# Optimization experiments

Hardware: AMD Instinct MI355X
Metric: run time of the kernel (lower is better)

Reference implementation:

```python
import jax, jax.numpy as jnp
import numpy as np

EPS = 1e-5  # torch BatchNorm1d default eps
N0, N, ORIG, F, K, H, NC = 16, 96, 92, 64, 41, 128, 3


def _bn(x, g, b, axes):
    # training-mode batchnorm: biased batch stats over `axes`, per-channel affine
    m = jnp.mean(x, axis=axes, keepdims=True)
    v = jnp.mean((x - m) ** 2, axis=axes, keepdims=True)
    return (x - m) / jnp.sqrt(v + EPS) * g + b


def setup_inputs() -> dict:
    key = jax.random.key(0)
    ks = jax.random.split(key, 16)
    s = 0.05
    return {
        "atom_fea": jax.random.normal(ks[0], (N0, N, ORIG), jnp.float32),
        "nbr_fea": jax.random.normal(ks[1], (N0, N, N, K), jnp.float32),
        "adj": jax.random.randint(ks[2], (N0, N, N), 0, 2, jnp.int64),
        "emb_W": jax.random.normal(ks[3], (ORIG, F), jnp.float32) * s,
        "emb_b": jnp.zeros((F,), jnp.float32),
        "conv_W": jax.random.normal(ks[4], (NC, 2 * F + K, 2 * F), jnp.float32) * s,
        "conv_b": jnp.zeros((NC, 2 * F), jnp.float32),
        "bn1_g": jnp.ones((NC, 2 * F), jnp.float32),
        "bn1_b": jnp.zeros((NC, 2 * F), jnp.float32),
        "bn2_g": jnp.ones((NC, F), jnp.float32),
        "bn2_b": jnp.zeros((NC, F), jnp.float32),
        "fc_W": jax.random.normal(ks[5], (F, H), jnp.float32) * s,
        "fc_b": jnp.zeros((H,), jnp.float32),
        "out_W": jax.random.normal(ks[6], (H, 1), jnp.float32) * s,
        "out_b": jnp.zeros((1,), jnp.float32),
    }


def reference(atom_fea, nbr_fea, adj, emb_W, emb_b, conv_W, conv_b,
              bn1_g, bn1_b, bn2_g, bn2_b, fc_W, fc_b, out_W, out_b):
    fea = atom_fea @ emb_W + emb_b                       # (N0, N, F)
    adjf = adj.astype(fea.dtype)[..., None]              # (N0, N, N, 1)
    for i in range(NC):
        # NOTE: faithful to source - both FEA and masked term broadcast atom j's
        # own features along the neighbor axis (unsqueeze(2) in torch code).
        FEA = jnp.broadcast_to(fea[:, :, None, :], (N0, N, N, F))
        total = jnp.concatenate([FEA, adjf * FEA, nbr_fea], axis=3)   # (N0,N,N,2F+K)
        gated = total @ conv_W[i] + conv_b[i]                         # (N0,N,N,2F)
        gated = _bn(gated, bn1_g[i], bn1_b[i], (0, 1, 2))
        filt, core = jnp.split(gated, 2, axis=3)
        summed = jnp.sum(jax.nn.sigmoid(filt) * jax.nn.softplus(core), axis=2)  # (N0,N,F)
        summed = _bn(summed, bn2_g[i], bn2_b[i], (0, 1))
        fea = jax.nn.softplus(fea + summed)
    crys = jnp.mean(fea, axis=1)                                      # (N0, F)
    crys = jax.nn.softplus(jax.nn.softplus(crys) @ fc_W + fc_b)       # (N0, H)
    return crys @ out_W + out_b                                       # (N0, 1)
```

## Files before the change

### kernel.cpp

```cpp
#include <hip/hip_runtime.h>
#include <math.h>

#define N0c   16
#define NAt   96
#define ORIG  92
#define Fc    64
#define Kc    41
#define Hc    128
#define NCc   3
#define C2    128
#define EPSBN 1e-5f
#define JG    4
#define JPW   (NAt / JG)
#define NREP  32
#define SRL_STRIDE 12288
#define AROW  72
#define WFRAG 16384
#define INV1  (1.f / (float)(N0c * NAt * NAt))
#define INV2  (1.f / (float)(N0c * NAt))

typedef __attribute__((ext_vector_type(8))) short short8_t;
typedef __attribute__((ext_vector_type(4))) float f32x4;

__device__ __forceinline__ float sp_(float x){
    return fmaxf(x, 0.f) + __logf(1.f + __expf(-fabsf(x)));
}
__device__ __forceinline__ float sgm_(float x){
    return 1.f / (1.f + __expf(-x));
}
__device__ __forceinline__ unsigned short bfhi(float x){
    union { float f; unsigned u; } v; v.f = x;
    unsigned r = v.u + 0x7fff + ((v.u >> 16) & 1);
    return (unsigned short)(r >> 16);
}
__device__ __forceinline__ float bf2f(unsigned short h){
    union { float f; unsigned u; } v; v.u = ((unsigned)h) << 16; return v.f;
}

__global__ __launch_bounds__(256) void k_pre(const float* __restrict__ nbr,
                                             const int*   __restrict__ adj,
                                             float* __restrict__ ST,
                                             float* __restrict__ cntf){
    int r    = blockIdx.x;
    int lane = threadIdx.x & 63;
    int jg   = __builtin_amdgcn_readfirstlane(threadIdx.x >> 6);
    __shared__ float rS[JG][Kc], rT[JG][Kc], rc[JG];
    float S = 0.f, T = 0.f, cn = 0.f;
    int j0 = jg * JPW;
    for (int j = j0; j < j0 + JPW; ++j){
        float a = (float)adj[r * NAt + j];
        float v = (lane < Kc) ? nbr[((size_t)r * NAt + j) * Kc + lane] : 0.f;
        S += v; T += a * v; cn += a;
    }
    if (lane < Kc){ rS[jg][lane] = S; rT[jg][lane] = T; }
    if (lane == 0) rc[jg] = cn;
    __syncthreads();
    int t = threadIdx.x;
    if (t < Kc){
        ST[r * (2 * Kc) + t]      = rS[0][t] + rS[1][t] + rS[2][t] + rS[3][t];
        ST[r * (2 * Kc) + Kc + t] = rT[0][t] + rT[1][t] + rT[2][t] + rT[3][t];
    }
    if (t == 0) cntf[r] = rc[0] + rc[1] + rc[2] + rc[3];
}

__global__ __launch_bounds__(128) void k_gram(const float* __restrict__ nbr,
                                              const int*   __restrict__ adj,
                                              float* __restrict__ pG,
                                              float* __restrict__ ST,
                                              float* __restrict__ cntf,
                                              float* __restrict__ G,
                                              int rpb, int doST){
    int blk = blockIdx.x;
    int t   = threadIdx.x;
    int k   = (t % 21) * 2;
    int lb  = (t / 21) * 7;
    __shared__ float L[NAt * Kc];
    __shared__ float AJf[NAt];
    if (blk == 0){
        for (int i = t; i < Kc * Kc; i += 128) G[i] = 0.f;
    }
    float a0[7] = {0,0,0,0,0,0,0}, a1[7] = {0,0,0,0,0,0,0};
    for (int rr = 0; rr < rpb; ++rr){
        int r = blk * rpb + rr;
        __syncthreads();
        for (int i = t; i < NAt * Kc; i += 128)
            L[i] = nbr[(size_t)r * NAt * Kc + i];
        if (t < NAt) AJf[t] = (float)adj[r * NAt + t];
        __syncthreads();
        if (doST && t < Kc){
            float S = 0.f, T = 0.f;
            for (int j = 0; j < NAt; ++j){
                float v = L[j * Kc + t];
                S += v; T += AJf[j] * v;
            }
            ST[r * (2 * Kc) + t]      = S;
            ST[r * (2 * Kc) + Kc + t] = T;
        }
        if (doST && t == Kc){
            float cn = 0.f;
            for (int j = 0; j < NAt; ++j) cn += AJf[j];
            cntf[r] = cn;
        }
        if (t < 126){
            for (int j = 0; j < NAt; ++j){
                float vk0 = L[j * Kc + k];
                float vk1 = (k + 1 < Kc) ? L[j * Kc + k + 1] : 0.f;
                #pragma unroll
                for (int m = 0; m < 7; ++m){
                    if (lb + m < Kc){
                        float lv = L[j * Kc + lb + m];
                        a0[m] += vk0 * lv;
                        a1[m] += vk1 * lv;
                    }
                }
            }
        }
    }
    if (t < 126){
        float* dst = pG + (size_t)blk * (Kc * Kc);
        #pragma unroll
        for (int m = 0; m < 7; ++m){
            if (lb + m < Kc){
                dst[k * Kc + lb + m] = a0[m];
                if (k + 1 < Kc) dst[(k + 1) * Kc + lb + m] = a1[m];
            }
        }
    }
}

__global__ __launch_bounds__(64) void k_gred(const float* __restrict__ pG,
                                             float* __restrict__ G){
    int i  = (blockIdx.x % 27) * 64 + threadIdx.x;
    int b0 = (blockIdx.x / 27) * 96;
    if (i < Kc * Kc){
        float s = 0.f;
        #pragma unroll 4
        for (int b = b0; b < b0 + 96; ++b) s += pG[(size_t)b * (Kc * Kc) + i];
        atomicAdd(&G[i], s);
    }
}

__global__ __launch_bounds__(320) void k_prep(const float* __restrict__ G,
                                              const float* __restrict__ convW,
                                              float* __restrict__ W3T,
                                              unsigned short* __restrict__ W3F,
                                              float* __restrict__ q3){
    int bi   = blockIdx.x;
    int l    = bi >> 5;
    int g    = bi & 31;
    int tid  = threadIdx.x;
    int lane = tid & 63;
    int w    = __builtin_amdgcn_readfirstlane(tid >> 6);
    const float* Wl = convW + (size_t)l * 169 * C2;
    __shared__ float GL[Kc * Kc];
    __shared__ float w3s[4][Kc];
    for (int i = tid; i < Kc * Kc; i += 320) GL[i] = G[i];

    int   c  = g * 4 + (w & 3);
    float w3 = 0.f;
    if (w < 4){
        w3 = (lane < Kc) ? Wl[(C2 + lane) * C2 + c] : 0.f;
        if (lane < 44)
            W3T[((size_t)l * C2 + c) * 44 + lane] = (lane < Kc) ? w3 : 0.f;
        if (lane < Kc) w3s[w][lane] = w3;
    }
    __syncthreads();

    if (w == 4){
        int h  = g & 1;
        int ks = (g >> 1) & 1;
        int nt = g >> 2;
        int n  = nt * 16 + (lane & 15);
        unsigned short* dst = W3F + (size_t)l * WFRAG + g * 512 + lane * 8;
        #pragma unroll
        for (int i = 0; i < 8; ++i){
            int kk = ks * 32 + (lane >> 4) * 8 + i;
            float x = (kk < Kc) ? Wl[(C2 + kk) * C2 + n] : 0.f;
            unsigned short hi = bfhi(x);
            dst[i] = h ? bfhi(x - bf2f(hi)) : hi;
        }
    } else {
        float gw = 0.f;
        if (lane < Kc){
            #pragma unroll
            for (int m = 0; m < Kc; ++m) gw += GL[lane * Kc + m] * w3s[w][m];
        }
        float part = (lane < Kc) ? w3 * gw : 0.f;
        part += __shfl_xor(part, 1);
        part += __shfl_xor(part, 2);
        part += __shfl_xor(part, 4);
        part += __shfl_xor(part, 8);
        part += __shfl_xor(part, 16);
        part += __shfl_xor(part, 32);
        if (lane == 0) q3[l * C2 + c] = part;
    }
}

__global__ __launch_bounds__(256)
void k_front(float* __restrict__ fea,
             const float* __restrict__ atom,
             const float* __restrict__ embW,
             const float* __restrict__ embB,
             const float* __restrict__ Wl,
             const float* __restrict__ bl,
             const float* __restrict__ W3Tl,
             const float* __restrict__ ST,
             const float* __restrict__ cntf,
             float* __restrict__ p1,
             float* __restrict__ p2,
             float* __restrict__ sum1R,
             float* __restrict__ sq1R,
             const float* __restrict__ summed,
             const float* __restrict__ sum2Rp,
             const float* __restrict__ sq2Rp,
             const float* __restrict__ g2p,
             const float* __restrict__ b2p,
             int upd){
    int r    = blockIdx.x;
    int tid  = threadIdx.x;
    int c    = tid & 127;
    int half = __builtin_amdgcn_readfirstlane(tid >> 7);
    __shared__ float F[Fc];
    __shared__ float A2L[Fc], B2L[Fc];
    __shared__ float P1h[C2], P2h[C2], TTs[C2];

    if (upd){
        if (tid < Fc){
            float s = 0.f, q = 0.f;
            for (int rr = 0; rr < NREP; ++rr){
                s += sum2Rp[rr * Fc + tid];
                q += sq2Rp[rr * Fc + tid];
            }
            float m = s * INV2;
            float v = q * INV2 - m * m;
            float A = g2p[tid] * rsqrtf(v + EPSBN);
            A2L[tid] = A;
            B2L[tid] = b2p[tid] - m * A;
        }
        __syncthreads();
        if (tid < Fc){
            float nv = sp_(fea[r * Fc + tid] + summed[r * Fc + tid] * A2L[tid] + B2L[tid]);
            F[tid] = nv;
            fea[r * Fc + tid] = nv;
        }
        __syncthreads();
    } else {
        if (tid < Fc){
            const float* ar = atom + r * ORIG;
            float acc = embB[tid];
            #pragma unroll 4
            for (int o = 0; o < ORIG; ++o) acc += ar[o] * embW[o * Fc + tid];
            F[tid] = acc;
            fea[r * Fc + tid] = acc;
        }
        __syncthreads();
    }

    float a1p = 0.f, a2p = 0.f;
    int f0 = half * 32;
    #pragma unroll 8
    for (int f = f0; f < f0 + 32; ++f){
        float fv = F[f];
        a1p += fv * Wl[f * C2 + c];
        a2p += fv * Wl[(Fc + f) * C2 + c];
    }
    const float* wt = W3Tl + c * 44;
    const float* Sr = ST + r * (2 * Kc) + half * Kc;
    float dot = 0.f;
    #pragma unroll
    for (int k = 0; k < 40; k += 4){
        float4 wv = *(const float4*)(wt + k);
        dot += Sr[k] * wv.x + Sr[k + 1] * wv.y + Sr[k + 2] * wv.z + Sr[k + 3] * wv.w;
    }
    dot += Sr[40] * wt[40];

    if (half == 1){ P1h[c] = a1p; P2h[c] = a2p; TTs[c] = dot; }
    __syncthreads();
    if (half == 0){
        float a1 = a1p + P1h[c] + bl[c];
        float a2 = a2p + P2h[c];
        float u  = dot;
        float tt = TTs[c];
        p1[r * C2 + c] = a1;
        p2[r * C2 + c] = a2;
        float cn = cntf[r];
        float s1 = (float)NAt * a1 + cn * a2 + u;
        float q1 = (float)NAt * a1 * a1 + cn * a2 * a2
                 + 2.f * cn * a1 * a2 + 2.f * a1 * u + 2.f * a2 * tt;
        int slot = blockIdx.x & (NREP - 1);
        atomicAdd(&sum1R[slot * C2 + c], s1);
        atomicAdd(&sq1R[slot * C2 + c], q1);
    }
}

__global__ __launch_bounds__(512)
void k_apply(const float* __restrict__ nbr,
             const int*   __restrict__ adj,
             const unsigned short* __restrict__ W3Fl,
             const float* __restrict__ p1,
             const float* __restrict__ p2,
             const float* __restrict__ sum1R,
             const float* __restrict__ sq1R,
             const float* __restrict__ qv,
             const float* __restrict__ g1,
             const float* __restrict__ b1,
             float* __restrict__ summed,
             float* __restrict__ sum2R,
             float* __restrict__ sq2R){
    int r    = blockIdx.x;
    int tid  = threadIdx.x;
    int lane = tid & 63;
    int w    = __builtin_amdgcn_readfirstlane(tid >> 6);
    int ntF  = w & 3;
    int mh   = w >> 2;

    __shared__ unsigned short sAH[NAt * AROW];
    __shared__ unsigned short sAL[NAt * AROW];
    __shared__ float AJ[NAt];
    __shared__ float PL1[C2], PL2[C2], A1L[C2], B1L[C2];
    __shared__ float TpW[8][16];

    short8_t BH[2][2], BL[2][2];
    #pragma unroll
    for (int ni = 0; ni < 2; ++ni){
        int nt = ntF + ni * 4;
        #pragma unroll
        for (int ks = 0; ks < 2; ++ks){
            int fidH = (nt * 2 + ks) * 2;
            BH[ni][ks] = *(const short8_t*)(W3Fl + fidH * 512 + lane * 8);
            BL[ni][ks] = *(const short8_t*)(W3Fl + (fidH + 1) * 512 + lane * 8);
        }
    }

    const float* nb = nbr + (size_t)r * (NAt * Kc);
    for (int idx = tid; idx < NAt * Kc; idx += 512){
        int j = idx / Kc, k = idx - j * Kc;
        float x = nb[idx];
        unsigned short hi = bfhi(x);
        sAH[j * AROW + k] = hi;
        sAL[j * AROW + k] = bfhi(x - bf2f(hi));
    }
    for (int idx = tid; idx < NAt * 23; idx += 512){
        int j = idx / 23, k = Kc + (idx - j * 23);
        sAH[j * AROW + k] = 0;
        sAL[j * AROW + k] = 0;
    }
    if (tid < C2){
        int c = tid;
        float s = 0.f, q = 0.f;
        for (int rr = 0; rr < NREP; ++rr){ s += sum1R[rr * C2 + c]; q += sq1R[rr * C2 + c]; }
        float m = s * INV1;
        float v = (q + qv[c]) * INV1 - m * m;
        float A = g1[c] * rsqrtf(v + EPSBN);
        A1L[c] = A;
        B1L[c] = b1[c] - m * A;
    } else if (tid < 256){
        PL1[tid - 128] = p1[r * C2 + tid - 128];
    } else if (tid < 384){
        PL2[tid - 256] = p2[r * C2 + tid - 256];
    } else if (tid < 480){
        AJ[tid - 384] = (float)adj[r * NAt + tid - 384];
    }
    __syncthreads();

    f32x4 acc[3][2] = {};
    int q4 = (lane >> 4) * 8;
    #pragma unroll
    for (int mt = 0; mt < 3; ++mt){
        int jrow = (mh * 48 + mt * 16 + (lane & 15)) * AROW;
        short8_t AH0 = *(const short8_t*)(&sAH[jrow + q4]);
        short8_t AH1 = *(const short8_t*)(&sAH[jrow + 32 + q4]);
        short8_t AL0 = *(const short8_t*)(&sAL[jrow + q4]);
        short8_t AL1 = *(const short8_t*)(&sAL[jrow + 32 + q4]);
        #pragma unroll
        for (int ni = 0; ni < 2; ++ni){
            acc[mt][ni] = __builtin_amdgcn_mfma_f32_16x16x32_bf16(AH0, BH[ni][0], acc[mt][ni], 0, 0, 0);
            acc[mt][ni] = __builtin_amdgcn_mfma_f32_16x16x32_bf16(AH0, BL[ni][0], acc[mt][ni], 0, 0, 0);
            acc[mt][ni] = __builtin_amdgcn_mfma_f32_16x16x32_bf16(AL0, BH[ni][0], acc[mt][ni], 0, 0, 0);
            acc[mt][ni] = __builtin_amdgcn_mfma_f32_16x16x32_bf16(AH1, BH[ni][1], acc[mt][ni], 0, 0, 0);
            acc[mt][ni] = __builtin_amdgcn_mfma_f32_16x16x32_bf16(AH1, BL[ni][1], acc[mt][ni], 0, 0, 0);
            acc[mt][ni] = __builtin_amdgcn_mfma_f32_16x16x32_bf16(AL1, BH[ni][1], acc[mt][ni], 0, 0, 0);
        }
    }

    int cF = ntF * 16 + (lane & 15);
    int cC = cF + 64;
    float p1F = PL1[cF], p2F = PL2[cF], A1F = A1L[cF], B1F = B1L[cF];
    float p1C = PL1[cC], p2C = PL2[cC], A1C = A1L[cC], B1C = B1L[cC];
    float tsum = 0.f;
    #pragma unroll
    for (int mt = 0; mt < 3; ++mt){
        #pragma unroll
        for (int rg = 0; rg < 4; ++rg){
            int j = mh * 48 + mt * 16 + (lane >> 4) * 4 + rg;
            float ajf = AJ[j];
            float gf = (p1F + ajf * p2F + acc[mt][0][rg]) * A1F + B1F;
            float gc = (p1C + ajf * p2C + acc[mt][1][rg]) * A1C + B1C;
            tsum += sgm_(gf) * sp_(gc);
        }
    }
    tsum += __shfl_xor(tsum, 16);
    tsum += __shfl_xor(tsum, 32);
    if (lane < 16) TpW[w][lane] = tsum;
    __syncthreads();
    if (tid < Fc){
        int f = tid;
        float s = TpW[f >> 4][f & 15] + TpW[(f >> 4) + 4][f & 15];
        summed[r * Fc + f] = s;
        int slot = blockIdx.x & (NREP - 1);
        atomicAdd(&sum2R[slot * Fc + f], s);
        atomicAdd(&sq2R[slot * Fc + f], s * s);
    }
}

__global__ __launch_bounds__(128) void k_final(const float* __restrict__ fea,
                                               const float* __restrict__ summed,
                                               const float* __restrict__ sum2R,
                                               const float* __restrict__ sq2R,
                                               const float* __restrict__ g2,
                                               const float* __restrict__ b2,
                                               const float* __restrict__ fcW,
                                               const float* __restrict__ fcb,
                                               const float* __restrict__ outW,
                                               const float* __restrict__ outb,
                                               float* __restrict__ out){
    int b = blockIdx.x;
    int t = threadIdx.x;
    __shared__ float spc[Fc];
    __shared__ float red[Hc];
    if (t < Fc){
        float s = 0.f, q = 0.f;
        for (int r = 0; r < NREP; ++r){ s += sum2R[r * Fc + t]; q += sq2R[r * Fc + t]; }
        float m  = s * INV2;
        float v  = q * INV2 - m * m;
        float A2 = g2[t] * rsqrtf(v + EPSBN);
        float B2 = b2[t] - m * A2;
        float acc = 0.f;
        for (int i = 0; i < NAt; ++i){
            int idx = (b * NAt + i) * Fc + t;
            acc += sp_(fea[idx] + summed[idx] * A2 + B2);
        }
        spc[t] = sp_(acc * (1.f / NAt));
    }
    __syncthreads();
    float h = fcb[t];
    #pragma unroll 4
    for (int f = 0; f < Fc; ++f) h += spc[f] * fcW[f * Hc + t];
    h = sp_(h);
    red[t] = h * outW[t];
    __syncthreads();
    for (int off = 64; off > 0; off >>= 1){
        if (t < off) red[t] += red[t + off];
        __syncthreads();
    }
    if (t == 0) out[b] = red[0] + outb[0];
}

extern "C" void kernel_launch(void* const* d_in, const int* in_sizes, int n_in,
                              void* d_out, int out_size, void* d_ws, size_t ws_size,
                              hipStream_t stream){
    const float* atom  = (const float*)d_in[0];
    const float* nbr   = (const float*)d_in[1];
    const int*   adj   = (const int*)  d_in[2];
    const float* embW  = (const float*)d_in[3];
    const float* embB  = (const float*)d_in[4];
    const float* convW = (const float*)d_in[5];
    const float* convB = (const float*)d_in[6];
    const float* bn1g  = (const float*)d_in[7];
    const float* bn1b  = (const float*)d_in[8];
    const float* bn2g  = (const float*)d_in[9];
    const float* bn2b  = (const float*)d_in[10];
    const float* fcW   = (const float*)d_in[11];
    const float* fcb   = (const float*)d_in[12];
    const float* outW  = (const float*)d_in[13];
    const float* outb  = (const float*)d_in[14];
    float* out = (float*)d_out;
    float* ws  = (float*)d_ws;

    const int ROWS = N0c * NAt;
    float* fea    = ws;
    float* p1     = ws + 98304;
    float* p2     = ws + 294912;
    float* summed = ws + 491520;
    float* SRL    = ws + 589824;
    float* ST     = ws + 626688;
    float* cntf   = ws + 752640;
    float* q3     = ws + 754176;
    float* W3T    = ws + 754560;
    unsigned short* W3F = (unsigned short*)(ws + 771456);
    const size_t PERS = 796032;

    size_t ws_f = ws_size / sizeof(float);
    int nblk; float *pG, *G; int compact = 0;
    if (ws_f >= PERS + (size_t)1536 * 1681 + 1681 + 64){
        nblk = 1536; pG = ws + PERS; G = pG + (size_t)nblk * 1681;
    } else if (ws_f >= PERS + (size_t)768 * 1681 + 1681 + 64){
        nblk = 768;  pG = ws + PERS; G = pG + (size_t)nblk * 1681;
    } else if (ws_f >= PERS + (size_t)384 * 1681 + 1681 + 64){
        nblk = 384;  pG = ws + PERS; G = pG + (size_t)nblk * 1681;
    } else {
        nblk = 384;  pG = ws;        G = ws + 650000;  compact = 1;
    }
    int rpb = 1536 / nblk;
    int ph  = nblk / 96;

    k_gram <<<nblk, 128, 0, stream>>>(nbr, adj, pG, ST, cntf, G, rpb,
                                      compact ? 0 : 1);
    k_gred <<<27 * ph, 64, 0, stream>>>(pG, G);
    k_prep <<<NCc * 32, 320, 0, stream>>>(G, convW, W3T, W3F, q3);
    if (compact)
        k_pre <<<ROWS, 256, 0, stream>>>(nbr, adj, ST, cntf);
    hipMemsetAsync(SRL, 0, 3 * SRL_STRIDE * sizeof(float), stream);

    for (int l = 0; l < NCc; ++l){
        const float* Wl   = convW + (size_t)l * 169 * C2;
        const float* bl   = convB + l * C2;
        const float* W3Tl = W3T + (size_t)l * C2 * 44;
        const unsigned short* W3Fl = W3F + (size_t)l * WFRAG;
        float* sum1R = SRL + l * SRL_STRIDE;
        float* sq1R  = sum1R + 4096;
        float* sum2R = sum1R + 8192;
        float* sq2R  = sum1R + 10240;
        const float* sum2Rp = (l > 0) ? SRL + (l - 1) * SRL_STRIDE + 8192 : SRL;
        const float* sq2Rp  = (l > 0) ? SRL + (l - 1) * SRL_STRIDE + 10240 : SRL;
        const float* g2p    = bn2g + (l > 0 ? (l - 1) : 0) * Fc;
        const float* b2p    = bn2b + (l > 0 ? (l - 1) : 0) * Fc;

        k_front <<<ROWS, 256, 0, stream>>>(fea, atom, embW, embB,
                                           Wl, bl, W3Tl, ST, cntf,
                                           p1, p2, sum1R, sq1R,
                                           summed, sum2Rp, sq2Rp, g2p, b2p,
                                           l > 0 ? 1 : 0);
        k_apply <<<ROWS, 512, 0, stream>>>(nbr, adj, W3Fl, p1, p2,
                                           sum1R, sq1R, q3 + l * C2,
                                           bn1g + l * C2, bn1b + l * C2,
                                           summed, sum2R, sq2R);
    }

    k_final<<<N0c, Hc, 0, stream>>>(fea, summed,
                                    SRL + 2 * SRL_STRIDE + 8192,
                                    SRL + 2 * SRL_STRIDE + 10240,
                                    bn2g + 2 * Fc, bn2b + 2 * Fc,
                                    fcW, fcb, outW, outb, out);
}
```

Baseline: 263.0 us.

## Fuse per-layer front/apply kernels into one persistent kernel with grid barriers

Replaces the seven per-layer k_front/k_apply launches and k_final with a single persistent kernel of 256 blocks, each owning 6 rows. Layers are separated by atomic-counter grid barriers, and per-row features, p1/p2 and summed stay in shared memory instead of going through global memory. This removes launch overhead and intermediate round-trips. In exchange it runs far fewer blocks, so there is less parallelism and less latency hiding, and correctness depends on all 256 blocks being co-resident.

```diff
diff --git a/kernel.cpp b/kernel.cpp
--- a/kernel.cpp
+++ b/kernel.cpp
@@ -18,6 +18,8 @@
 #define WFRAG 16384
 #define INV1  (1.f / (float)(N0c * NAt * NAt))
 #define INV2  (1.f / (float)(N0c * NAt))
+#define NBLK  256
+#define RPB   6
 
 typedef __attribute__((ext_vector_type(8))) short short8_t;
 typedef __attribute__((ext_vector_type(4))) float f32x4;
@@ -35,6 +37,18 @@
 }
 __device__ __forceinline__ float bf2f(unsigned short h){
     union { float f; unsigned u; } v; v.u = ((unsigned)h) << 16; return v.f;
+}
+
+__device__ __forceinline__ void gbar(unsigned* __restrict__ bar, int slot){
+    __syncthreads();
+    if (threadIdx.x == 0){
+        __threadfence();
+        atomicAdd(&bar[slot], 1u);
+        while (atomicAdd(&bar[slot], 0u) < (unsigned)NBLK)
+            __builtin_amdgcn_s_sleep(2);
+    }
+    __syncthreads();
+    __threadfence();
 }
 
 __global__ __launch_bounds__(256) void k_pre(const float* __restrict__ nbr,
@@ -196,264 +210,287 @@
     }
 }
 
-__global__ __launch_bounds__(256)
-void k_front(float* __restrict__ fea,
-             const float* __restrict__ atom,
-             const float* __restrict__ embW,
-             const float* __restrict__ embB,
-             const float* __restrict__ Wl,
-             const float* __restrict__ bl,
-             const float* __restrict__ W3Tl,
-             const float* __restrict__ ST,
-             const float* __restrict__ cntf,
-             float* __restrict__ p1,
-             float* __restrict__ p2,
-             float* __restrict__ sum1R,
-             float* __restrict__ sq1R,
-             const float* __restrict__ summed,
-             const float* __restrict__ sum2Rp,
-             const float* __restrict__ sq2Rp,
-             const float* __restrict__ g2p,
-             const float* __restrict__ b2p,
-             int upd){
-    int r    = blockIdx.x;
-    int tid  = threadIdx.x;
-    int c    = tid & 127;
-    int half = __builtin_amdgcn_readfirstlane(tid >> 7);
-    __shared__ float F[Fc];
-    __shared__ float A2L[Fc], B2L[Fc];
-    __shared__ float P1h[C2], P2h[C2], TTs[C2];
-
-    if (upd){
-        if (tid < Fc){
-            float s = 0.f, q = 0.f;
-            for (int rr = 0; rr < NREP; ++rr){
-                s += sum2Rp[rr * Fc + tid];
-                q += sq2Rp[rr * Fc + tid];
-            }
-            float m = s * INV2;
-            float v = q * INV2 - m * m;
-            float A = g2p[tid] * rsqrtf(v + EPSBN);
-            A2L[tid] = A;
-            B2L[tid] = b2p[tid] - m * A;
-        }
-        __syncthreads();
-        if (tid < Fc){
-            float nv = sp_(fea[r * Fc + tid] + summed[r * Fc + tid] * A2L[tid] + B2L[tid]);
-            F[tid] = nv;
-            fea[r * Fc + tid] = nv;
-        }
-        __syncthreads();
-    } else {
-        if (tid < Fc){
-            const float* ar = atom + r * ORIG;
-            float acc = embB[tid];
-            #pragma unroll 4
-            for (int o = 0; o < ORIG; ++o) acc += ar[o] * embW[o * Fc + tid];
-            F[tid] = acc;
-            fea[r * Fc + tid] = acc;
-        }
-        __syncthreads();
-    }
-
-    float a1p = 0.f, a2p = 0.f;
-    int f0 = half * 32;
-    #pragma unroll 8
-    for (int f = f0; f < f0 + 32; ++f){
-        float fv = F[f];
-        a1p += fv * Wl[f * C2 + c];
-        a2p += fv * Wl[(Fc + f) * C2 + c];
-    }
-    const float* wt = W3Tl + c * 44;
-    const float* Sr = ST + r * (2 * Kc) + half * Kc;
-    float dot = 0.f;
-    #pragma unroll
-    for (int k = 0; k < 40; k += 4){
-        float4 wv = *(const float4*)(wt + k);
-        dot += Sr[k] * wv.x + Sr[k + 1] * wv.y + Sr[k + 2] * wv.z + Sr[k + 3] * wv.w;
-    }
-    dot += Sr[40] * wt[40];
-
-    if (half == 1){ P1h[c] = a1p; P2h[c] = a2p; TTs[c] = dot; }
-    __syncthreads();
-    if (half == 0){
-        float a1 = a1p + P1h[c] + bl[c];
-        float a2 = a2p + P2h[c];
-        float u  = dot;
-        float tt = TTs[c];
-        p1[r * C2 + c] = a1;
-        p2[r * C2 + c] = a2;
-        float cn = cntf[r];
-        float s1 = (float)NAt * a1 + cn * a2 + u;
-        float q1 = (float)NAt * a1 * a1 + cn * a2 * a2
-                 + 2.f * cn * a1 * a2 + 2.f * a1 * u + 2.f * a2 * tt;
-        int slot = blockIdx.x & (NREP - 1);
-        atomicAdd(&sum1R[slot * C2 + c], s1);
-        atomicAdd(&sq1R[slot * C2 + c], q1);
-    }
-}
-
 __global__ __launch_bounds__(512)
-void k_apply(const float* __restrict__ nbr,
-             const int*   __restrict__ adj,
-             const unsigned short* __restrict__ W3Fl,
-             const float* __restrict__ p1,
-             const float* __restrict__ p2,
-             const float* __restrict__ sum1R,
-             const float* __restrict__ sq1R,
-             const float* __restrict__ qv,
-             const float* __restrict__ g1,
-             const float* __restrict__ b1,
-             float* __restrict__ summed,
-             float* __restrict__ sum2R,
-             float* __restrict__ sq2R){
-    int r    = blockIdx.x;
-    int tid  = threadIdx.x;
-    int lane = tid & 63;
-    int w    = __builtin_amdgcn_readfirstlane(tid >> 6);
-    int ntF  = w & 3;
-    int mh   = w >> 2;
+void k_mega(const float* __restrict__ nbr,
+            const int*   __restrict__ adj,
+            const float* __restrict__ atom,
+            const float* __restrict__ embW,
+            const float* __restrict__ embB,
+            const float* __restrict__ convW,
+            const float* __restrict__ convB,
+            const float* __restrict__ W3T,
+            const unsigned short* __restrict__ W3F,
+            const float* __restrict__ q3,
+            const float* __restrict__ ST,
+            const float* __restrict__ cntf,
+            const float* __restrict__ bn1g,
+            const float* __restrict__ bn1b,
+            const float* __restrict__ bn2g,
+            const float* __restrict__ bn2b,
+            const float* __restrict__ fcW,
+            const float* __restrict__ fcb,
+            const float* __restrict__ outW,
+            const float* __restrict__ outb,
+            float* __restrict__ fea,
+            float* __restrict__ summed,
+            float* __restrict__ SRL,
+            unsigned* __restrict__ bar,
+            float* __restrict__ out){
+    int b     = blockIdx.x;
+    int tid   = threadIdx.x;
+    int rbase = b * RPB;
+    int lane  = tid & 63;
+    int w     = __builtin_amdgcn_readfirstlane(tid >> 6);
 
     __shared__ unsigned short sAH[NAt * AROW];
     __shared__ unsigned short sAL[NAt * AROW];
+    __shared__ float FEs[RPB][Fc];
+    __shared__ float P1s[RPB][C2], P2s[RPB][C2];
+    __shared__ float SMs[RPB][Fc];
+    __shared__ float A1L[C2], B1L[C2], A2L[Fc], B2L[Fc];
     __shared__ float AJ[NAt];
-    __shared__ float PL1[C2], PL2[C2], A1L[C2], B1L[C2];
     __shared__ float TpW[8][16];
-
-    short8_t BH[2][2], BL[2][2];
-    #pragma unroll
-    for (int ni = 0; ni < 2; ++ni){
-        int nt = ntF + ni * 4;
-        #pragma unroll
-        for (int ks = 0; ks < 2; ++ks){
-            int fidH = (nt * 2 + ks) * 2;
-            BH[ni][ks] = *(const short8_t*)(W3Fl + fidH * 512 + lane * 8);
-            BL[ni][ks] = *(const short8_t*)(W3Fl + (fidH + 1) * 512 + lane * 8);
-        }
-    }
-
-    const float* nb = nbr + (size_t)r * (NAt * Kc);
-    for (int idx = tid; idx < NAt * Kc; idx += 512){
-        int j = idx / Kc, k = idx - j * Kc;
-        float x = nb[idx];
-        unsigned short hi = bfhi(x);
-        sAH[j * AROW + k] = hi;
-        sAL[j * AROW + k] = bfhi(x - bf2f(hi));
-    }
+    __shared__ float P1h[2][C2], P2h[2][C2], TTs[2][C2];
+    __shared__ float spc[Fc], red[Hc];
+
     for (int idx = tid; idx < NAt * 23; idx += 512){
         int j = idx / 23, k = Kc + (idx - j * 23);
         sAH[j * AROW + k] = 0;
         sAL[j * AROW + k] = 0;
     }
-    if (tid < C2){
-        int c = tid;
-        float s = 0.f, q = 0.f;
-        for (int rr = 0; rr < NREP; ++rr){ s += sum1R[rr * C2 + c]; q += sq1R[rr * C2 + c]; }
-        float m = s * INV1;
-        float v = (q + qv[c]) * INV1 - m * m;
-        float A = g1[c] * rsqrtf(v + EPSBN);
-        A1L[c] = A;
-        B1L[c] = b1[c] - m * A;
-    } else if (tid < 256){
-        PL1[tid - 128] = p1[r * C2 + tid - 128];
-    } else if (tid < 384){
-        PL2[tid - 256] = p2[r * C2 + tid - 256];
-    } else if (tid < 480){
-        AJ[tid - 384] = (float)adj[r * NAt + tid - 384];
-    }
-    __syncthreads();
-
-    f32x4 acc[3][2] = {};
-    int q4 = (lane >> 4) * 8;
-    #pragma unroll
-    for (int mt = 0; mt < 3; ++mt){
-        int jrow = (mh * 48 + mt * 16 + (lane & 15)) * AROW;
-        short8_t AH0 = *(const short8_t*)(&sAH[jrow + q4]);
-        short8_t AH1 = *(const short8_t*)(&sAH[jrow + 32 + q4]);
-        short8_t AL0 = *(const short8_t*)(&sAL[jrow + q4]);
-        short8_t AL1 = *(const short8_t*)(&sAL[jrow + 32 + q4]);
+
+    int grp  = tid >> 8;
+    int tt   = tid & 255;
+    int c    = tt & 127;
+    int half = tt >> 7;
+
+    for (int l = 0; l < NCc; ++l){
+        const float* Wl   = convW + (size_t)l * 169 * C2;
+        const float* blp  = convB + l * C2;
+        const float* W3Tl = W3T + (size_t)l * C2 * 44;
+        float* sum1R = SRL + l * SRL_STRIDE;
+        float* sq1R  = sum1R + 4096;
+        float* sum2R = sum1R + 8192;
+        float* sq2R  = sum1R + 10240;
+
+        if (l > 0){
+            const float* sum2Rp = SRL + (l - 1) * SRL_STRIDE + 8192;
+            const float* sq2Rp  = sum2Rp + 2048;
+            const float* g2p    = bn2g + (l - 1) * Fc;
+            const float* b2p    = bn2b + (l - 1) * Fc;
+            if (tid < Fc){
+                float s = 0.f, q = 0.f;
+                for (int rr = 0; rr < NREP; ++rr){
+                    s += sum2Rp[rr * Fc + tid];
+                    q += sq2Rp[rr * Fc + tid];
+                }
+                float m = s * INV2;
+                float v = q * INV2 - m * m;
+                float A = g2p[tid] * rsqrtf(v + EPSBN);
+                A2L[tid] = A;
+                B2L[tid] = b2p[tid] - m * A;
+            }
+        }
+        __syncthreads();
+
+        for (int sub = 0; sub < RPB / 2; ++sub){
+            int ri = sub * 2 + grp;
+            int r  = rbase + ri;
+            if (tt < Fc){
+                float nv;
+                if (l > 0){
+                    nv = sp_(FEs[ri][tt] + SMs[ri][tt] * A2L[tt] + B2L[tt]);
+                } else {
+                    const float* ar = atom + r * ORIG;
+                    float acc = embB[tt];
+                    #pragma unroll 4
+                    for (int o = 0; o < ORIG; ++o) acc += ar[o] * embW[o * Fc + tt];
+                    nv = acc;
+                }
+                FEs[ri][tt] = nv;
+                if (l == NCc - 1) fea[r * Fc + tt] = nv;
+            }
+            __syncthreads();
+
+            float a1p = 0.f, a2p = 0.f;
+            int f0 = half * 32;
+            #pragma unroll 8
+            for (int f = f0; f < f0 + 32; ++f){
+                float fv = FEs[ri][f];
+                a1p += fv * Wl[f * C2 + c];
+                a2p += fv * Wl[(Fc + f) * C2 + c];
+            }
+            const float* wt = W3Tl + c * 44;
+            const float* Sr = ST + r * (2 * Kc) + half * Kc;
+            float dot = 0.f;
+            #pragma unroll
+            for (int k = 0; k < 40; k += 4){
+                float4 wv = *(const float4*)(wt + k);
+                dot += Sr[k] * wv.x + Sr[k + 1] * wv.y + Sr[k + 2] * wv.z + Sr[k + 3] * wv.w;
+            }
+            dot += Sr[40] * wt[40];
+
+            if (half == 1){ P1h[grp][c] = a1p; P2h[grp][c] = a2p; TTs[grp][c] = dot; }
+            __syncthreads();
+            if (half == 0){
+                float a1  = a1p + P1h[grp][c] + blp[c];
+                float a2  = a2p + P2h[grp][c];
+                float u   = dot;
+                float ttv = TTs[grp][c];
+                P1s[ri][c] = a1;
+                P2s[ri][c] = a2;
+                float cn = cntf[r];
+                float s1 = (float)NAt * a1 + cn * a2 + u;
+                float q1 = (float)NAt * a1 * a1 + cn * a2 * a2
+                         + 2.f * cn * a1 * a2 + 2.f * a1 * u + 2.f * a2 * ttv;
+                int slot = b & (NREP - 1);
+                atomicAdd(&sum1R[slot * C2 + c], s1);
+                atomicAdd(&sq1R[slot * C2 + c], q1);
+            }
+            __syncthreads();
+        }
+        gbar(bar, l * 2);
+
+        const unsigned short* W3Fl = W3F + (size_t)l * WFRAG;
+        int ntF = w & 3;
+        int mh  = w >> 2;
+        short8_t BH[2][2], BL[2][2];
         #pragma unroll
         for (int ni = 0; ni < 2; ++ni){
-            acc[mt][ni] = __builtin_amdgcn_mfma_f32_16x16x32_bf16(AH0, BH[ni][0], acc[mt][ni], 0, 0, 0);
-            acc[mt][ni] = __builtin_amdgcn_mfma_f32_16x16x32_bf16(AH0, BL[ni][0], acc[mt][ni], 0, 0, 0);
-            acc[mt][ni] = __builtin_amdgcn_mfma_f32_16x16x32_bf16(AL0, BH[ni][0], acc[mt][ni], 0, 0, 0);
-            acc[mt][ni] = __builtin_amdgcn_mfma_f32_16x16x32_bf16(AH1, BH[ni][1], acc[mt][ni], 0, 0, 0);
-            acc[mt][ni] = __builtin_amdgcn_mfma_f32_16x16x32_bf16(AH1, BL[ni][1], acc[mt][ni], 0, 0, 0);
-            acc[mt][ni] = __builtin_amdgcn_mfma_f32_16x16x32_bf16(AL1, BH[ni][1], acc[mt][ni], 0, 0, 0);
-        }
-    }
-
-    int cF = ntF * 16 + (lane & 15);
-    int cC = cF + 64;
-    float p1F = PL1[cF], p2F = PL2[cF], A1F = A1L[cF], B1F = B1L[cF];
-    float p1C = PL1[cC], p2C = PL2[cC], A1C = A1L[cC], B1C = B1L[cC];
-    float tsum = 0.f;
-    #pragma unroll
-    for (int mt = 0; mt < 3; ++mt){
-        #pragma unroll
-        for (int rg = 0; rg < 4; ++rg){
-            int j = mh * 48 + mt * 16 + (lane >> 4) * 4 + rg;
-            float ajf = AJ[j];
-            float gf = (p1F + ajf * p2F + acc[mt][0][rg]) * A1F + B1F;
-            float gc = (p1C + ajf * p2C + acc[mt][1][rg]) * A1C + B1C;
-            tsum += sgm_(gf) * sp_(gc);
-        }
-    }
-    tsum += __shfl_xor(tsum, 16);
-    tsum += __shfl_xor(tsum, 32);
-    if (lane < 16) TpW[w][lane] = tsum;
-    __syncthreads();
-    if (tid < Fc){
-        int f = tid;
-        float s = TpW[f >> 4][f & 15] + TpW[(f >> 4) + 4][f & 15];
-        summed[r * Fc + f] = s;
-        int slot = blockIdx.x & (NREP - 1);
-        atomicAdd(&sum2R[slot * Fc + f], s);
-        atomicAdd(&sq2R[slot * Fc + f], s * s);
-    }
-}
-
-__global__ __launch_bounds__(128) void k_final(const float* __restrict__ fea,
-                                               const float* __restrict__ summed,
-                                               const float* __restrict__ sum2R,
-                                               const float* __restrict__ sq2R,
-                                               const float* __restrict__ g2,
-                                               const float* __restrict__ b2,
-                                               const float* __restrict__ fcW,
-                                               const float* __restrict__ fcb,
-                                               const float* __restrict__ outW,
-                                               const float* __restrict__ outb,
-                                               float* __restrict__ out){
-    int b = blockIdx.x;
-    int t = threadIdx.x;
-    __shared__ float spc[Fc];
-    __shared__ float red[Hc];
-    if (t < Fc){
-        float s = 0.f, q = 0.f;
-        for (int r = 0; r < NREP; ++r){ s += sum2R[r * Fc + t]; q += sq2R[r * Fc + t]; }
-        float m  = s * INV2;
-        float v  = q * INV2 - m * m;
-        float A2 = g2[t] * rsqrtf(v + EPSBN);
-        float B2 = b2[t] - m * A2;
-        float acc = 0.f;
-        for (int i = 0; i < NAt; ++i){
-            int idx = (b * NAt + i) * Fc + t;
-            acc += sp_(fea[idx] + summed[idx] * A2 + B2);
-        }
-        spc[t] = sp_(acc * (1.f / NAt));
-    }
-    __syncthreads();
-    float h = fcb[t];
-    #pragma unroll 4
-    for (int f = 0; f < Fc; ++f) h += spc[f] * fcW[f * Hc + t];
-    h = sp_(h);
-    red[t] = h * outW[t];
-    __syncthreads();
-    for (int off = 64; off > 0; off >>= 1){
-        if (t < off) red[t] += red[t + off];
-        __syncthreads();
-    }
-    if (t == 0) out[b] = red[0] + outb[0];
+            int nt = ntF + ni * 4;
+            #pragma unroll
+            for (int ks = 0; ks < 2; ++ks){
+                int fidH = (nt * 2 + ks) * 2;
+                BH[ni][ks] = *(const short8_t*)(W3Fl + fidH * 512 + lane * 8);
+                BL[ni][ks] = *(const short8_t*)(W3Fl + (fidH + 1) * 512 + lane * 8);
+            }
+        }
+        if (tid < C2){
+            int cc = tid;
+            float s = 0.f, qq = 0.f;
+            for (int rr = 0; rr < NREP; ++rr){
+                s += sum1R[rr * C2 + cc]; qq += sq1R[rr * C2 + cc];
+            }
+            float m = s * INV1;
+            float v = (qq + q3[l * C2 + cc]) * INV1 - m * m;
+            float A = bn1g[l * C2 + cc] * rsqrtf(v + EPSBN);
+            A1L[cc] = A;
+            B1L[cc] = bn1b[l * C2 + cc] - m * A;
+        }
+        __syncthreads();
+
+        for (int ri = 0; ri < RPB; ++ri){
+            int r = rbase + ri;
+            const float* nb = nbr + (size_t)r * (NAt * Kc);
+            for (int idx = tid; idx < NAt * Kc; idx += 512){
+                int j = idx / Kc, k = idx - j * Kc;
+                float x = nb[idx];
+                unsigned short hi = bfhi(x);
+                sAH[j * AROW + k] = hi;
+                sAL[j * AROW + k] = bfhi(x - bf2f(hi));
+            }
+            if (tid < NAt) AJ[tid] = (float)adj[r * NAt + tid];
+            __syncthreads();
+
+            f32x4 acc[3][2] = {};
+            int q4 = (lane >> 4) * 8;
+            #pragma unroll
+            for (int mt = 0; mt < 3; ++mt){
+                int jrow = (mh * 48 + mt * 16 + (lane & 15)) * AROW;
+                short8_t AH0 = *(const short8_t*)(&sAH[jrow + q4]);
+                short8_t AH1 = *(const short8_t*)(&sAH[jrow + 32 + q4]);
+                short8_t AL0 = *(const short8_t*)(&sAL[jrow + q4]);
+                short8_t AL1 = *(const short8_t*)(&sAL[jrow + 32 + q4]);
+                #pragma unroll
+                for (int ni = 0; ni < 2; ++ni){
+                    acc[mt][ni] = __builtin_amdgcn_mfma_f32_16x16x32_bf16(AH0, BH[ni][0], acc[mt][ni], 0, 0, 0);
+                    acc[mt][ni] = __builtin_amdgcn_mfma_f32_16x16x32_bf16(AH0, BL[ni][0], acc[mt][ni], 0, 0, 0);
+                    acc[mt][ni] = __builtin_amdgcn_mfma_f32_16x16x32_bf16(AL0, BH[ni][0], acc[mt][ni], 0, 0, 0);
+                    acc[mt][ni] = __builtin_amdgcn_mfma_f32_16x16x32_bf16(AH1, BH[ni][1], acc[mt][ni], 0, 0, 0);
+                    acc[mt][ni] = __builtin_amdgcn_mfma_f32_16x16x32_bf16(AH1, BL[ni][1], acc[mt][ni], 0, 0, 0);
+                    acc[mt][ni] = __builtin_amdgcn_mfma_f32_16x16x32_bf16(AL1, BH[ni][1], acc[mt][ni], 0, 0, 0);
+                }
+            }
+
+            int cF = ntF * 16 + (lane & 15);
+            int cC = cF + 64;
+            float p1F = P1s[ri][cF], p2F = P2s[ri][cF], A1F = A1L[cF], B1F = B1L[cF];
+            float p1C = P1s[ri][cC], p2C = P2s[ri][cC], A1C = A1L[cC], B1C = B1L[cC];
+            float tsum = 0.f;
+            #pragma unroll
+            for (int mt = 0; mt < 3; ++mt){
+                #pragma unroll
+                for (int rg = 0; rg < 4; ++rg){
+                    int j = mh * 48 + mt * 16 + (lane >> 4) * 4 + rg;
+                    float ajf = AJ[j];
+                    float gf = (p1F + ajf * p2F + acc[mt][0][rg]) * A1F + B1F;
+                    float gc = (p1C + ajf * p2C + acc[mt][1][rg]) * A1C + B1C;
+                    tsum += sgm_(gf) * sp_(gc);
+                }
+            }
+            tsum += __shfl_xor(tsum, 16);
+            tsum += __shfl_xor(tsum, 32);
+            if (lane < 16) TpW[w][lane] = tsum;
+            __syncthreads();
+            if (tid < Fc){
+                float s = TpW[tid >> 4][tid & 15] + TpW[(tid >> 4) + 4][tid & 15];
+                SMs[ri][tid] = s;
+                if (l == NCc - 1) summed[r * Fc + tid] = s;
+                int slot = b & (NREP - 1);
+                atomicAdd(&sum2R[slot * Fc + tid], s);
+                atomicAdd(&sq2R[slot * Fc + tid], s * s);
+            }
+            __syncthreads();
+        }
+        gbar(bar, l * 2 + 1);
+    }
+
+    if (b < N0c){
+        const float* sum2R = SRL + 2 * SRL_STRIDE + 8192;
+        const float* sq2R  = sum2R + 2048;
+        const float* g2 = bn2g + 2 * Fc;
+        const float* b2 = bn2b + 2 * Fc;
+        if (tid < Fc){
+            float s = 0.f, q = 0.f;
+            for (int rr = 0; rr < NREP; ++rr){
+                s += sum2R[rr * Fc + tid]; q += sq2R[rr * Fc + tid];
+            }
+            float m  = s * INV2;
+            float v  = q * INV2 - m * m;
+            float A2 = g2[tid] * rsqrtf(v + EPSBN);
+            A2L[tid] = A2;
+            B2L[tid] = b2[tid] - m * A2;
+        }
+        __syncthreads();
+        int tg = tid >> 7, t2 = tid & 127;
+        if (t2 < Fc){
+            float accp = 0.f;
+            for (int i = tg * 24; i < tg * 24 + 24; ++i){
+                int idx = (b * NAt + i) * Fc + t2;
+                accp += sp_(fea[idx] + summed[idx] * A2L[t2] + B2L[t2]);
+            }
+            P1s[tg][t2] = accp;
+        }
+        __syncthreads();
+        if (tid < Fc){
+            float acc = P1s[0][tid] + P1s[1][tid] + P1s[2][tid] + P1s[3][tid];
+            spc[tid] = sp_(acc * (1.f / NAt));
+        }
+        __syncthreads();
+        if (tid < Hc){
+            float h = fcb[tid];
+            #pragma unroll 4
+            for (int f = 0; f < Fc; ++f) h += spc[f] * fcW[f * Hc + tid];
+            h = sp_(h);
+            red[tid] = h * outW[tid];
+        }
+        __syncthreads();
+        for (int off = 64; off > 0; off >>= 1){
+            if (tid < off) red[tid] += red[tid + off];
+            __syncthreads();
+        }
+        if (tid == 0) out[b] = red[0] + outb[0];
+    }
 }
 
 extern "C" void kernel_launch(void* const* d_in, const int* in_sizes, int n_in,
@@ -479,8 +516,7 @@
 
     const int ROWS = N0c * NAt;
     float* fea    = ws;
-    float* p1     = ws + 98304;
-    float* p2     = ws + 294912;
+    unsigned* bar = (unsigned*)(ws + 98304);
     float* summed = ws + 491520;
     float* SRL    = ws + 589824;
     float* ST     = ws + 626688;
@@ -511,35 +547,11 @@
     if (compact)
         k_pre <<<ROWS, 256, 0, stream>>>(nbr, adj, ST, cntf);
     hipMemsetAsync(SRL, 0, 3 * SRL_STRIDE * sizeof(float), stream);
-
-    for (int l = 0; l < NCc; ++l){
-        const float* Wl   = convW + (size_t)l * 169 * C2;
-        const float* bl   = convB + l * C2;
-        const float* W3Tl = W3T + (size_t)l * C2 * 44;
-        const unsigned short* W3Fl = W3F + (size_t)l * WFRAG;
-        float* sum1R = SRL + l * SRL_STRIDE;
-        float* sq1R  = sum1R + 4096;
-        float* sum2R = sum1R + 8192;
-        float* sq2R  = sum1R + 10240;
-        const float* sum2Rp = (l > 0) ? SRL + (l - 1) * SRL_STRIDE + 8192 : SRL;
-        const float* sq2Rp  = (l > 0) ? SRL + (l - 1) * SRL_STRIDE + 10240 : SRL;
-        const float* g2p    = bn2g + (l > 0 ? (l - 1) : 0) * Fc;
-        const float* b2p    = bn2b + (l > 0 ? (l - 1) : 0) * Fc;
-
-        k_front <<<ROWS, 256, 0, stream>>>(fea, atom, embW, embB,
-                                           Wl, bl, W3Tl, ST, cntf,
-                                           p1, p2, sum1R, sq1R,
-                                           summed, sum2Rp, sq2Rp, g2p, b2p,
-                                           l > 0 ? 1 : 0);
-        k_apply <<<ROWS, 512, 0, stream>>>(nbr, adj, W3Fl, p1, p2,
-                                           sum1R, sq1R, q3 + l * C2,
-                                           bn1g + l * C2, bn1b + l * C2,
-                                           summed, sum2R, sq2R);
-    }
-
-    k_final<<<N0c, Hc, 0, stream>>>(fea, summed,
-                                    SRL + 2 * SRL_STRIDE + 8192,
-                                    SRL + 2 * SRL_STRIDE + 10240,
-                                    bn2g + 2 * Fc, bn2b + 2 * Fc,
-                                    fcW, fcb, outW, outb, out);
-}
+    hipMemsetAsync(bar, 0, 64 * sizeof(unsigned), stream);
+
+    k_mega <<<NBLK, 512, 0, stream>>>(nbr, adj, atom, embW, embB, convW, convB,
+                                      W3T, W3F, q3, ST, cntf,
+                                      bn1g, bn1b, bn2g, bn2b,
+                                      fcW, fcb, outW, outb,
+                                      fea, summed, SRL, bar, out);
+}
```

After: 652.9 us. +148.3%, slower.
